# Kernel tuning notes

Measured on AMD Instinct MI355X. Metric: run time of the kernel, lower is better.

## Reference

```python
import jax, jax.numpy as jnp
import numpy as np

SEQ, B, CIN, H, K = 2048, 16, 512, 512, 2

def setup_inputs() -> dict:
    key = jax.random.key(0)
    k1, k2, k3 = jax.random.split(key, 3)
    x = jax.random.normal(k1, (SEQ, B, CIN), dtype=jnp.float32)
    W = jax.random.normal(k2, (3 * H, CIN, K), dtype=jnp.float32) * (1.0 / np.sqrt(CIN * K))
    b = jax.random.normal(k3, (3 * H,), dtype=jnp.float32) * 0.01
    return {"x": x, "W": W, "b": b}

def _qrnn_fo(x, W, b):
    # x: (T, B, Cin) -> conv input (B, Cin, T), causal left pad of K-1 zeros
    xb = jnp.transpose(x, (1, 2, 0))
    g = jax.lax.conv_general_dilated(
        xb, W, window_strides=(1,), padding=[(K - 1, 0)],
        dimension_numbers=("NCH", "OIH", "NCH"))
    g = g + b[None, :, None]
    g = jnp.transpose(g, (2, 0, 1))  # (T, B, 3H)
    zg, fg, og = jnp.split(g, 3, axis=-1)
    z = jnp.tanh(zg)
    f = jax.nn.sigmoid(fg)
    o = jax.nn.sigmoid(og)

    def step(c, gates_t):
        zt, ft, ot = gates_t
        c = ft * c + (1.0 - ft) * zt
        h = c * ot
        return c, h

    c0 = jnp.zeros((B, H), dtype=x.dtype)
    c_last, hs = jax.lax.scan(step, c0, (z, f, o))
    return hs, c_last

def reference(x, W, b):
    hs, c_last = _qrnn_fo(x, W, b)
    h_last = hs[-1]
    return hs, h_last[None, :], c_last[None, :]
```

## Files before the change

kernel.cpp:

```cpp
#include <hip/hip_runtime.h>

#define SEQ   2048
#define BATCH 16
#define CINCH 512
#define HDIM  512
#define NDIM  1536
#define TBM   (SEQ*BATCH)
#define KRED  1024
#define NCH   32
#define CHL   64
#define NCOL  8192

typedef unsigned short ushort_t;
typedef __bf16 bf16x8 __attribute__((ext_vector_type(8)));
typedef unsigned short u16x8 __attribute__((ext_vector_type(8)));
typedef float f32x4 __attribute__((ext_vector_type(4)));

__device__ __forceinline__ float bf2f(ushort_t u) {
    return __uint_as_float(((unsigned int)u) << 16);
}
__device__ __forceinline__ ushort_t f2bf(float x) {
    unsigned int u = __float_as_uint(x);
    unsigned int r = u + 0x7fffu + ((u >> 16) & 1u);
    return (ushort_t)(r >> 16);
}

__global__ void cast_x_kernel(const float* __restrict__ x, ushort_t* __restrict__ xb) {
    int i = blockIdx.x * 256 + threadIdx.x;
    int e = i * 4;
    ushort4 r;
    if (e < BATCH * CINCH) {
        r.x = 0; r.y = 0; r.z = 0; r.w = 0;
    } else {
        float4 v = *(const float4*)(x + (e - BATCH * CINCH));
        r.x = f2bf(v.x); r.y = f2bf(v.y); r.z = f2bf(v.z); r.w = f2bf(v.w);
    }
    *(ushort4*)(xb + e) = r;
}

__global__ void repack_w_kernel(const float* __restrict__ W, ushort_t* __restrict__ wb) {
    int i = blockIdx.x * 256 + threadIdx.x;
    int o  = i >> 10;
    int r  = i & 1023;
    int k  = r >> 9;
    int ci = r & 511;
    wb[i] = f2bf(W[o * 1024 + ci * 2 + k]);
}

__device__ __forceinline__ void load_lds_16B(const ushort_t* g, ushort_t* l) {
    auto* gp = reinterpret_cast<const __attribute__((address_space(1))) unsigned int*>(
        reinterpret_cast<uintptr_t>(g));
    auto* lp = reinterpret_cast<__attribute__((address_space(3))) unsigned int*>(
        reinterpret_cast<uintptr_t>(l));
    __builtin_amdgcn_global_load_lds(gp, lp, 16, 0, 0);
}

__global__ __launch_bounds__(256) void gemm_gates_kernel(
    const ushort_t* __restrict__ xb, const ushort_t* __restrict__ wb,
    const float* __restrict__ bias,
    ushort_t* __restrict__ zb, ushort_t* __restrict__ fb, ushort_t* __restrict__ ob) {

    __shared__ ushort_t smem[2 * 128 * 64];
    ushort_t* As = smem;
    ushort_t* Bs = smem + 128 * 64;

    const int tid  = threadIdx.x;
    const int w    = tid >> 6;
    const int lane = tid & 63;
    const int quad = lane >> 4;
    const int l15  = lane & 15;
    const int wm   = w & 1;
    const int wn   = w >> 1;
    const int mBase = blockIdx.x * 128;
    const int nBase = blockIdx.y * 128;

    const int srow = lane >> 3;
    const int scb  = lane & 7;

    f32x4 acc[4][4];
#pragma unroll
    for (int i = 0; i < 4; ++i)
#pragma unroll
        for (int j = 0; j < 4; ++j)
            acc[i][j] = (f32x4){0.f, 0.f, 0.f, 0.f};

    for (int kt = 0; kt < 16; ++kt) {
        __syncthreads();
        const long aOff = (kt < 8) ? (long)kt * 64 : (long)16 * 512 + (long)(kt - 8) * 64;
#pragma unroll
        for (int i = 0; i < 4; ++i) {
            const int row = w * 32 + i * 8 + srow;
            const int cbd = scb ^ (row & 7);
            const ushort_t* ga = xb + (long)(mBase + row) * 512 + aOff + cbd * 8;
            load_lds_16B(ga, &As[(w * 32 + i * 8) * 64]);
            const ushort_t* gb = wb + (long)(nBase + row) * 1024 + kt * 64 + cbd * 8;
            load_lds_16B(gb, &Bs[(w * 32 + i * 8) * 64]);
        }
        __syncthreads();

#pragma unroll
        for (int ks = 0; ks < 2; ++ks) {
            bf16x8 af[4], bfr[4];
            const int cbd = ks * 4 + quad;
#pragma unroll
            for (int mt = 0; mt < 4; ++mt) {
                int ml  = wm * 64 + mt * 16 + l15;
                int off = ml * 64 + ((cbd ^ (ml & 7)) * 8);
                af[mt] = __builtin_bit_cast(bf16x8, *(const u16x8*)(&As[off]));
            }
#pragma unroll
            for (int nt = 0; nt < 4; ++nt) {
                int nl  = wn * 64 + nt * 16 + l15;
                int off = nl * 64 + ((cbd ^ (nl & 7)) * 8);
                bfr[nt] = __builtin_bit_cast(bf16x8, *(const u16x8*)(&Bs[off]));
            }
#pragma unroll
            for (int mt = 0; mt < 4; ++mt)
#pragma unroll
                for (int nt = 0; nt < 4; ++nt)
                    acc[mt][nt] = __builtin_amdgcn_mfma_f32_16x16x32_bf16(
                        af[mt], bfr[nt], acc[mt][nt], 0, 0, 0);
        }
    }

    const int gate = nBase >> 9;
    const int hb   = nBase & 511;

    __syncthreads();
#pragma unroll
    for (int nt = 0; nt < 4; ++nt) {
        const int n_local = wn * 64 + nt * 16 + l15;
        const float bv = bias[nBase + n_local];
#pragma unroll
        for (int mt = 0; mt < 4; ++mt) {
#pragma unroll
            for (int r = 0; r < 4; ++r) {
                const int m_local = wm * 64 + mt * 16 + quad * 4 + r;
                float g = acc[mt][nt][r] + bv;
                float a;
                if (gate == 0) {
                    float e = __expf(-2.f * fabsf(g));
                    float t = (1.f - e) / (1.f + e);
                    a = copysignf(t, g);
                } else {
                    a = 1.f / (1.f + __expf(-g));
                }
                const int phys = ((n_local >> 3) ^ (m_local & 7)) * 8 + (n_local & 7);
                smem[m_local * 128 + phys] = f2bf(a);
            }
        }
    }
    __syncthreads();

    ushort_t* outp = (gate == 0) ? zb : (gate == 1) ? fb : ob;
#pragma unroll
    for (int s = 0; s < 8; ++s) {
        const int m_local = w * 32 + s * 4 + quad;
        const int blk = l15 ^ (m_local & 7);
        u16x8 v = *(const u16x8*)(&smem[m_local * 128 + blk * 8]);
        *(u16x8*)(outp + (long)(mBase + m_local) * 512 + hb + l15 * 8) = v;
    }
}

__global__ __launch_bounds__(256) void scan_compose(
    const ushort_t* __restrict__ zb, const ushort_t* __restrict__ fb,
    float* __restrict__ Acomp, float* __restrict__ Bcomp) {
    const int col = (blockIdx.x & 31) * 256 + threadIdx.x;
    const int ch  = blockIdx.x >> 5;
    const long base = (long)ch * CHL * NCOL + col;
    float A = 1.f, Bv = 0.f;
    const int U = 16;
    for (int w0 = 0; w0 < CHL; w0 += U) {
        float zc[U], fc[U];
#pragma unroll
        for (int u = 0; u < U; ++u) {
            long idx = base + (long)(w0 + u) * NCOL;
            zc[u] = bf2f(zb[idx]); fc[u] = bf2f(fb[idx]);
        }
#pragma unroll
        for (int u = 0; u < U; ++u) {
            Bv = fc[u] * Bv + (1.f - fc[u]) * zc[u];
            A *= fc[u];
        }
    }
    Acomp[ch * NCOL + col] = A;
    Bcomp[ch * NCOL + col] = Bv;
}

__global__ void scan_prefix(const float* __restrict__ Acomp,
                            const float* __restrict__ Bcomp,
                            float* __restrict__ Cin) {
    const int col = blockIdx.x * 256 + threadIdx.x;
    float c = 0.f;
#pragma unroll 4
    for (int ch = 0; ch < NCH; ++ch) {
        Cin[ch * NCOL + col] = c;
        c = Acomp[ch * NCOL + col] * c + Bcomp[ch * NCOL + col];
    }
}

__global__ __launch_bounds__(256) void scan_apply(
    const ushort_t* __restrict__ zb, const ushort_t* __restrict__ fb,
    const ushort_t* __restrict__ ob, const float* __restrict__ Cin,
    float* __restrict__ out) {
    const int col = (blockIdx.x & 31) * 256 + threadIdx.x;
    const int ch  = blockIdx.x >> 5;
    const long base = (long)ch * CHL * NCOL + col;
    float c = Cin[ch * NCOL + col];
    float h = 0.f;
    const int U = 16;
    for (int w0 = 0; w0 < CHL; w0 += U) {
        float zc[U], fc[U], oc[U];
#pragma unroll
        for (int u = 0; u < U; ++u) {
            long idx = base + (long)(w0 + u) * NCOL;
            zc[u] = bf2f(zb[idx]); fc[u] = bf2f(fb[idx]); oc[u] = bf2f(ob[idx]);
        }
#pragma unroll
        for (int u = 0; u < U; ++u) {
            c = fc[u] * c + (1.f - fc[u]) * zc[u];
            h = c * oc[u];
            out[base + (long)(w0 + u) * NCOL] = h;
        }
    }
    if (ch == NCH - 1) {
        out[(long)SEQ * NCOL + col] = h;
        out[(long)SEQ * NCOL + NCOL + col] = c;
    }
}

extern "C" void kernel_launch(void* const* d_in, const int* in_sizes, int n_in,
                              void* d_out, int out_size, void* d_ws, size_t ws_size,
                              hipStream_t stream) {
    const float* x  = (const float*)d_in[0];
    const float* W  = (const float*)d_in[1];
    const float* bi = (const float*)d_in[2];
    float* out = (float*)d_out;

    char* ws = (char*)d_ws;
    const size_t xbN = (size_t)(TBM + BATCH) * CINCH;
    const size_t wbN = (size_t)NDIM * KRED;
    const size_t gN  = (size_t)TBM * HDIM;
    ushort_t* xb = (ushort_t*)ws;
    ushort_t* wb = (ushort_t*)(ws + xbN * 2);
    ushort_t* zb = (ushort_t*)(ws + xbN * 2 + wbN * 2);
    ushort_t* fb = zb + gN;
    ushort_t* ob = fb + gN;
    float* Acomp = (float*)ws;
    float* Bcomp = Acomp + NCH * NCOL;
    float* Cin   = Bcomp + NCH * NCOL;

    cast_x_kernel<<<16392, 256, 0, stream>>>(x, xb);
    repack_w_kernel<<<6144, 256, 0, stream>>>(W, wb);
    dim3 ggrid(TBM / 128, NDIM / 128);
    gemm_gates_kernel<<<ggrid, 256, 0, stream>>>(xb, wb, bi, zb, fb, ob);
    scan_compose<<<NCH * 32, 256, 0, stream>>>(zb, fb, Acomp, Bcomp);
    scan_prefix<<<NCOL / 256, 256, 0, stream>>>(Acomp, Bcomp, Cin);
    scan_apply<<<NCH * 32, 256, 0, stream>>>(zb, fb, ob, Cin, out);
}
```

Measured before the change: 296.0 us.

## Restructure gate GEMM into 256x256 double-buffered pipelined tiles and vectorize scans

The gate GEMM moves from 128x128 tiles with 4 waves to 256x256 tiles with 8 waves. It double-buffers A and B in 128KB of dynamic LDS, splits each K-step into four MFMA phases separated by barriers and s_setprio, and issues the loads for the next tile while the current one computes. The block index is remapped so consecutive blocks share rows and improve L2 reuse. The scan compose and apply kernels now process 4 columns per thread with ushort4 and float4 accesses, which widens memory transactions. The cost is heavier register pressure (32 accumulators per lane), a large LDS footprint that limits occupancy, and fewer blocks in the scan kernels.

```diff
diff --git a/kernel.cpp b/kernel.cpp
--- a/kernel.cpp
+++ b/kernel.cpp
@@ -55,136 +55,201 @@
     __builtin_amdgcn_global_load_lds(gp, lp, 16, 0, 0);
 }
 
-__global__ __launch_bounds__(256) void gemm_gates_kernel(
+__device__ __forceinline__ bf16x8 frag(const ushort_t* buf, int row, int cb) {
+    return __builtin_bit_cast(bf16x8,
+        *(const u16x8*)(&buf[row * 64 + ((cb ^ (row & 7)) * 8)]));
+}
+
+#define PHASE_BAR() do { __builtin_amdgcn_s_barrier(); asm volatile("" ::: "memory"); } while (0)
+
+__global__ __launch_bounds__(512, 2) void gemm_gates_kernel(
     const ushort_t* __restrict__ xb, const ushort_t* __restrict__ wb,
     const float* __restrict__ bias,
     ushort_t* __restrict__ zb, ushort_t* __restrict__ fb, ushort_t* __restrict__ ob) {
 
-    __shared__ ushort_t smem[2 * 128 * 64];
-    ushort_t* As = smem;
-    ushort_t* Bs = smem + 128 * 64;
+    extern __shared__ ushort_t smem[];
 
     const int tid  = threadIdx.x;
     const int w    = tid >> 6;
     const int lane = tid & 63;
     const int quad = lane >> 4;
     const int l15  = lane & 15;
-    const int wm   = w & 1;
-    const int wn   = w >> 1;
-    const int mBase = blockIdx.x * 128;
-    const int nBase = blockIdx.y * 128;
-
-    const int srow = lane >> 3;
-    const int scb  = lane & 7;
-
-    f32x4 acc[4][4];
-#pragma unroll
-    for (int i = 0; i < 4; ++i)
+    const int wm   = w >> 2;
+    const int wn   = w & 3;
+
+    const int wg    = (blockIdx.x & 7) * 96 + (blockIdx.x >> 3);
+    const int mBase = (wg / 6) * 256;
+    const int nBase = (wg % 6) * 256;
+
+    const int r0    = tid >> 3;
+    const int cbd   = (tid & 7) ^ (r0 & 7);
+    const int wbase = w * 8;
+
+    auto stageA = [&](ushort_t* dst, int u) {
+        const long aoff = (u < 8) ? (long)u * 64 : 8192L + (long)(u - 8) * 64;
+#pragma unroll
+        for (int ra = 0; ra < 4; ++ra) {
+            load_lds_16B(xb + (long)(mBase + ra * 64 + r0) * 512 + aoff + cbd * 8,
+                         dst + (ra * 64 + wbase) * 64);
+        }
+    };
+    auto stageB = [&](ushort_t* dst, int u) {
+        const long koff = (long)u * 64;
+#pragma unroll
+        for (int ra = 0; ra < 4; ++ra) {
+            load_lds_16B(wb + (long)(nBase + ra * 64 + r0) * 1024 + koff + cbd * 8,
+                         dst + (ra * 64 + wbase) * 64);
+        }
+    };
+
+    f32x4 acc[8][4];
+#pragma unroll
+    for (int i = 0; i < 8; ++i)
 #pragma unroll
         for (int j = 0; j < 4; ++j)
             acc[i][j] = (f32x4){0.f, 0.f, 0.f, 0.f};
 
-    for (int kt = 0; kt < 16; ++kt) {
-        __syncthreads();
-        const long aOff = (kt < 8) ? (long)kt * 64 : (long)16 * 512 + (long)(kt - 8) * 64;
-#pragma unroll
-        for (int i = 0; i < 4; ++i) {
-            const int row = w * 32 + i * 8 + srow;
-            const int cbd = scb ^ (row & 7);
-            const ushort_t* ga = xb + (long)(mBase + row) * 512 + aOff + cbd * 8;
-            load_lds_16B(ga, &As[(w * 32 + i * 8) * 64]);
-            const ushort_t* gb = wb + (long)(nBase + row) * 1024 + kt * 64 + cbd * 8;
-            load_lds_16B(gb, &Bs[(w * 32 + i * 8) * 64]);
-        }
-        __syncthreads();
-
-#pragma unroll
-        for (int ks = 0; ks < 2; ++ks) {
-            bf16x8 af[4], bfr[4];
-            const int cbd = ks * 4 + quad;
-#pragma unroll
-            for (int mt = 0; mt < 4; ++mt) {
-                int ml  = wm * 64 + mt * 16 + l15;
-                int off = ml * 64 + ((cbd ^ (ml & 7)) * 8);
-                af[mt] = __builtin_bit_cast(bf16x8, *(const u16x8*)(&As[off]));
-            }
-#pragma unroll
-            for (int nt = 0; nt < 4; ++nt) {
-                int nl  = wn * 64 + nt * 16 + l15;
-                int off = nl * 64 + ((cbd ^ (nl & 7)) * 8);
-                bfr[nt] = __builtin_bit_cast(bf16x8, *(const u16x8*)(&Bs[off]));
-            }
-#pragma unroll
-            for (int mt = 0; mt < 4; ++mt)
-#pragma unroll
-                for (int nt = 0; nt < 4; ++nt)
-                    acc[mt][nt] = __builtin_amdgcn_mfma_f32_16x16x32_bf16(
-                        af[mt], bfr[nt], acc[mt][nt], 0, 0, 0);
-        }
+    stageA(smem, 0);
+    stageB(smem + 32768, 0);
+    stageB(smem + 49152, 1);
+    asm volatile("s_waitcnt vmcnt(4)" ::: "memory");
+    PHASE_BAR();
+
+    int cur = 0;
+    for (int t = 0; t < 16; ++t) {
+        const ushort_t* cA = smem + cur * 16384;
+        const ushort_t* cB = smem + 32768 + cur * 16384;
+        bf16x8 a[4], b[4];
+
+#pragma unroll
+        for (int mt = 0; mt < 4; ++mt) a[mt] = frag(cA, wm * 128 + mt * 16 + l15, quad);
+#pragma unroll
+        for (int nt = 0; nt < 4; ++nt) b[nt] = frag(cB, wn * 64 + nt * 16 + l15, quad);
+        if (t < 15) stageA(smem + (cur ^ 1) * 16384, t + 1);
+        __builtin_amdgcn_s_setprio(1);
+#pragma unroll
+        for (int mt = 0; mt < 4; ++mt)
+#pragma unroll
+            for (int nt = 0; nt < 4; ++nt)
+                acc[mt][nt] = __builtin_amdgcn_mfma_f32_16x16x32_bf16(a[mt], b[nt], acc[mt][nt], 0, 0, 0);
+        __builtin_amdgcn_s_setprio(0);
+        PHASE_BAR();
+
+#pragma unroll
+        for (int mt = 0; mt < 4; ++mt) a[mt] = frag(cA, wm * 128 + (mt + 4) * 16 + l15, quad);
+        __builtin_amdgcn_s_setprio(1);
+#pragma unroll
+        for (int mt = 0; mt < 4; ++mt)
+#pragma unroll
+            for (int nt = 0; nt < 4; ++nt)
+                acc[mt + 4][nt] = __builtin_amdgcn_mfma_f32_16x16x32_bf16(a[mt], b[nt], acc[mt + 4][nt], 0, 0, 0);
+        __builtin_amdgcn_s_setprio(0);
+        PHASE_BAR();
+
+#pragma unroll
+        for (int mt = 0; mt < 4; ++mt) a[mt] = frag(cA, wm * 128 + mt * 16 + l15, 4 + quad);
+#pragma unroll
+        for (int nt = 0; nt < 4; ++nt) b[nt] = frag(cB, wn * 64 + nt * 16 + l15, 4 + quad);
+        __builtin_amdgcn_s_setprio(1);
+#pragma unroll
+        for (int mt = 0; mt < 4; ++mt)
+#pragma unroll
+            for (int nt = 0; nt < 4; ++nt)
+                acc[mt][nt] = __builtin_amdgcn_mfma_f32_16x16x32_bf16(a[mt], b[nt], acc[mt][nt], 0, 0, 0);
+        __builtin_amdgcn_s_setprio(0);
+        PHASE_BAR();
+
+#pragma unroll
+        for (int mt = 0; mt < 4; ++mt) a[mt] = frag(cA, wm * 128 + (mt + 4) * 16 + l15, 4 + quad);
+        __builtin_amdgcn_s_setprio(1);
+#pragma unroll
+        for (int mt = 0; mt < 4; ++mt)
+#pragma unroll
+            for (int nt = 0; nt < 4; ++nt)
+                acc[mt + 4][nt] = __builtin_amdgcn_mfma_f32_16x16x32_bf16(a[mt], b[nt], acc[mt + 4][nt], 0, 0, 0);
+        __builtin_amdgcn_s_setprio(0);
+        if (t < 14) {
+            stageB(smem + 32768 + cur * 16384, t + 2);
+            asm volatile("s_waitcnt vmcnt(4)" ::: "memory");
+        } else {
+            asm volatile("s_waitcnt vmcnt(0)" ::: "memory");
+        }
+        PHASE_BAR();
+        cur ^= 1;
     }
 
     const int gate = nBase >> 9;
     const int hb   = nBase & 511;
 
-    __syncthreads();
 #pragma unroll
     for (int nt = 0; nt < 4; ++nt) {
         const int n_local = wn * 64 + nt * 16 + l15;
         const float bv = bias[nBase + n_local];
 #pragma unroll
-        for (int mt = 0; mt < 4; ++mt) {
+        for (int mt = 0; mt < 8; ++mt) {
 #pragma unroll
             for (int r = 0; r < 4; ++r) {
-                const int m_local = wm * 64 + mt * 16 + quad * 4 + r;
+                const int m_local = wm * 128 + mt * 16 + quad * 4 + r;
                 float g = acc[mt][nt][r] + bv;
-                float a;
+                float av;
                 if (gate == 0) {
                     float e = __expf(-2.f * fabsf(g));
-                    float t = (1.f - e) / (1.f + e);
-                    a = copysignf(t, g);
+                    float tt = (1.f - e) / (1.f + e);
+                    av = copysignf(tt, g);
                 } else {
-                    a = 1.f / (1.f + __expf(-g));
+                    av = 1.f / (1.f + __expf(-g));
                 }
                 const int phys = ((n_local >> 3) ^ (m_local & 7)) * 8 + (n_local & 7);
-                smem[m_local * 128 + phys] = f2bf(a);
+                smem[m_local * 256 + phys] = f2bf(av);
             }
         }
     }
     __syncthreads();
 
     ushort_t* outp = (gate == 0) ? zb : (gate == 1) ? fb : ob;
-#pragma unroll
-    for (int s = 0; s < 8; ++s) {
-        const int m_local = w * 32 + s * 4 + quad;
-        const int blk = l15 ^ (m_local & 7);
-        u16x8 v = *(const u16x8*)(&smem[m_local * 128 + blk * 8]);
-        *(u16x8*)(outp + (long)(mBase + m_local) * 512 + hb + l15 * 8) = v;
-    }
+    const int lb    = tid & 31;
+    const int mrow0 = tid >> 5;
+#pragma unroll
+    for (int s = 0; s < 16; ++s) {
+        const int m_local = s * 16 + mrow0;
+        u16x8 v = *(const u16x8*)(&smem[m_local * 256 + ((lb ^ (m_local & 7)) * 8)]);
+        *(u16x8*)(outp + (long)(mBase + m_local) * 512 + hb + lb * 8) = v;
+    }
+}
+
+__device__ __forceinline__ void scan_step(float z, float f, float& A, float& Bv) {
+    Bv = f * Bv + (1.f - f) * z;
+    A *= f;
 }
 
 __global__ __launch_bounds__(256) void scan_compose(
     const ushort_t* __restrict__ zb, const ushort_t* __restrict__ fb,
     float* __restrict__ Acomp, float* __restrict__ Bcomp) {
-    const int col = (blockIdx.x & 31) * 256 + threadIdx.x;
-    const int ch  = blockIdx.x >> 5;
+    const int cg  = (blockIdx.x & 7) * 256 + threadIdx.x;
+    const int ch  = blockIdx.x >> 3;
+    const int col = cg * 4;
     const long base = (long)ch * CHL * NCOL + col;
-    float A = 1.f, Bv = 0.f;
-    const int U = 16;
+    float Ax = 1.f, Ay = 1.f, Az = 1.f, Aw = 1.f;
+    float Bx = 0.f, By = 0.f, Bz = 0.f, Bw = 0.f;
+    const int U = 8;
     for (int w0 = 0; w0 < CHL; w0 += U) {
-        float zc[U], fc[U];
+        ushort4 zr[U], fr[U];
 #pragma unroll
         for (int u = 0; u < U; ++u) {
-            long idx = base + (long)(w0 + u) * NCOL;
-            zc[u] = bf2f(zb[idx]); fc[u] = bf2f(fb[idx]);
+            const long idx = base + (long)(w0 + u) * NCOL;
+            zr[u] = *(const ushort4*)(zb + idx);
+            fr[u] = *(const ushort4*)(fb + idx);
         }
 #pragma unroll
         for (int u = 0; u < U; ++u) {
-            Bv = fc[u] * Bv + (1.f - fc[u]) * zc[u];
-            A *= fc[u];
-        }
-    }
-    Acomp[ch * NCOL + col] = A;
-    Bcomp[ch * NCOL + col] = Bv;
+            scan_step(bf2f(zr[u].x), bf2f(fr[u].x), Ax, Bx);
+            scan_step(bf2f(zr[u].y), bf2f(fr[u].y), Ay, By);
+            scan_step(bf2f(zr[u].z), bf2f(fr[u].z), Az, Bz);
+            scan_step(bf2f(zr[u].w), bf2f(fr[u].w), Aw, Bw);
+        }
+    }
+    *(float4*)(Acomp + (long)ch * NCOL + col) = make_float4(Ax, Ay, Az, Aw);
+    *(float4*)(Bcomp + (long)ch * NCOL + col) = make_float4(Bx, By, Bz, Bw);
 }
 
 __global__ void scan_prefix(const float* __restrict__ Acomp,
@@ -203,29 +268,36 @@
     const ushort_t* __restrict__ zb, const ushort_t* __restrict__ fb,
     const ushort_t* __restrict__ ob, const float* __restrict__ Cin,
     float* __restrict__ out) {
-    const int col = (blockIdx.x & 31) * 256 + threadIdx.x;
-    const int ch  = blockIdx.x >> 5;
+    const int cg  = (blockIdx.x & 7) * 256 + threadIdx.x;
+    const int ch  = blockIdx.x >> 3;
+    const int col = cg * 4;
     const long base = (long)ch * CHL * NCOL + col;
-    float c = Cin[ch * NCOL + col];
-    float h = 0.f;
-    const int U = 16;
+    float4 c0 = *(const float4*)(Cin + (long)ch * NCOL + col);
+    float cx = c0.x, cy = c0.y, cz = c0.z, cw = c0.w;
+    float hx = 0.f, hy = 0.f, hz = 0.f, hw = 0.f;
+    const int U = 8;
     for (int w0 = 0; w0 < CHL; w0 += U) {
-        float zc[U], fc[U], oc[U];
+        ushort4 zr[U], fr[U], orr[U];
 #pragma unroll
         for (int u = 0; u < U; ++u) {
-            long idx = base + (long)(w0 + u) * NCOL;
-            zc[u] = bf2f(zb[idx]); fc[u] = bf2f(fb[idx]); oc[u] = bf2f(ob[idx]);
+            const long idx = base + (long)(w0 + u) * NCOL;
+            zr[u]  = *(const ushort4*)(zb + idx);
+            fr[u]  = *(const ushort4*)(fb + idx);
+            orr[u] = *(const ushort4*)(ob + idx);
         }
 #pragma unroll
         for (int u = 0; u < U; ++u) {
-            c = fc[u] * c + (1.f - fc[u]) * zc[u];
-            h = c * oc[u];
-            out[base + (long)(w0 + u) * NCOL] = h;
+            float f, z;
+            f = bf2f(fr[u].x); z = bf2f(zr[u].x); cx = f * cx + (1.f - f) * z; hx = cx * bf2f(orr[u].x);
+            f = bf2f(fr[u].y); z = bf2f(zr[u].y); cy = f * cy + (1.f - f) * z; hy = cy * bf2f(orr[u].y);
+            f = bf2f(fr[u].z); z = bf2f(zr[u].z); cz = f * cz + (1.f - f) * z; hz = cz * bf2f(orr[u].z);
+            f = bf2f(fr[u].w); z = bf2f(zr[u].w); cw = f * cw + (1.f - f) * z; hw = cw * bf2f(orr[u].w);
+            *(float4*)(out + base + (long)(w0 + u) * NCOL) = make_float4(hx, hy, hz, hw);
         }
     }
     if (ch == NCH - 1) {
-        out[(long)SEQ * NCOL + col] = h;
-        out[(long)SEQ * NCOL + NCOL + col] = c;
+        *(float4*)(out + (long)SEQ * NCOL + col)        = make_float4(hx, hy, hz, hw);
+        *(float4*)(out + (long)SEQ * NCOL + NCOL + col) = make_float4(cx, cy, cz, cw);
     }
 }
 
@@ -250,11 +322,17 @@
     float* Bcomp = Acomp + NCH * NCOL;
     float* Cin   = Bcomp + NCH * NCOL;
 
+    static bool s_attr_set = false;
+    if (!s_attr_set) {
+        (void)hipFuncSetAttribute(reinterpret_cast<const void*>(&gemm_gates_kernel),
+                                  hipFuncAttributeMaxDynamicSharedMemorySize, 131072);
+        s_attr_set = true;
+    }
+
     cast_x_kernel<<<16392, 256, 0, stream>>>(x, xb);
     repack_w_kernel<<<6144, 256, 0, stream>>>(W, wb);
-    dim3 ggrid(TBM / 128, NDIM / 128);
-    gemm_gates_kernel<<<ggrid, 256, 0, stream>>>(xb, wb, bi, zb, fb, ob);
-    scan_compose<<<NCH * 32, 256, 0, stream>>>(zb, fb, Acomp, Bcomp);
+    gemm_gates_kernel<<<dim3(768), 512, 131072, stream>>>(xb, wb, bi, zb, fb, ob);
+    scan_compose<<<NCH * 8, 256, 0, stream>>>(zb, fb, Acomp, Bcomp);
     scan_prefix<<<NCOL / 256, 256, 0, stream>>>(Acomp, Bcomp, Cin);
-    scan_apply<<<NCH * 32, 256, 0, stream>>>(zb, fb, ob, Cin, out);
-}
+    scan_apply<<<NCH * 8, 256, 0, stream>>>(zb, fb, ob, Cin, out);
+}
```

Result: no change. 291.2 us (-1.6%).

## Load GEMM B fragments directly to registers and vectorize scan kernels by four columns

Applied to the files above, without the earlier changes.

The GEMM no longer stages the weight tile in LDS. Each lane loads its B fragments straight from global memory into registers, double-buffered across pairs of K steps, and only the A tile goes through LDS. This is meant to halve LDS traffic and shared memory use, possibly raising occupancy, at the cost of more VGPRs and uncoalesced global reads for B. The scan compose and apply kernels now process four columns per thread with ushort4/float4 accesses to cut instruction count. This leaves only 256 blocks per scan kernel, which may underfill the GPU.

```diff
diff --git a/kernel.cpp b/kernel.cpp
--- a/kernel.cpp
+++ b/kernel.cpp
@@ -55,14 +55,17 @@
     __builtin_amdgcn_global_load_lds(gp, lp, 16, 0, 0);
 }
 
+__device__ __forceinline__ bf16x8 bload(const ushort_t* p) {
+    return __builtin_bit_cast(bf16x8, *(const u16x8*)(p));
+}
+
 __global__ __launch_bounds__(256) void gemm_gates_kernel(
     const ushort_t* __restrict__ xb, const ushort_t* __restrict__ wb,
     const float* __restrict__ bias,
     ushort_t* __restrict__ zb, ushort_t* __restrict__ fb, ushort_t* __restrict__ ob) {
 
-    __shared__ ushort_t smem[2 * 128 * 64];
+    __shared__ ushort_t smem[128 * 128];
     ushort_t* As = smem;
-    ushort_t* Bs = smem + 128 * 64;
 
     const int tid  = threadIdx.x;
     const int w    = tid >> 6;
@@ -77,6 +80,8 @@
     const int srow = lane >> 3;
     const int scb  = lane & 7;
 
+    const ushort_t* bbase = wb + (long)(nBase + wn * 64 + l15) * 1024 + quad * 8;
+
     f32x4 acc[4][4];
 #pragma unroll
     for (int i = 0; i < 4; ++i)
@@ -84,23 +89,35 @@
         for (int j = 0; j < 4; ++j)
             acc[i][j] = (f32x4){0.f, 0.f, 0.f, 0.f};
 
-    for (int kt = 0; kt < 16; ++kt) {
+    bf16x8 bc0[4], bc1[4], bn0[4], bn1[4];
+
+#pragma unroll
+    for (int nt = 0; nt < 4; ++nt) {
+        bc0[nt] = bload(bbase + nt * 16384);
+        bc1[nt] = bload(bbase + nt * 16384 + 32);
+    }
+
+    for (int kt = 0; kt < 16; kt += 2) {
         __syncthreads();
-        const long aOff = (kt < 8) ? (long)kt * 64 : (long)16 * 512 + (long)(kt - 8) * 64;
-#pragma unroll
-        for (int i = 0; i < 4; ++i) {
-            const int row = w * 32 + i * 8 + srow;
-            const int cbd = scb ^ (row & 7);
-            const ushort_t* ga = xb + (long)(mBase + row) * 512 + aOff + cbd * 8;
-            load_lds_16B(ga, &As[(w * 32 + i * 8) * 64]);
-            const ushort_t* gb = wb + (long)(nBase + row) * 1024 + kt * 64 + cbd * 8;
-            load_lds_16B(gb, &Bs[(w * 32 + i * 8) * 64]);
+        {
+            const long aOff = (kt < 8) ? (long)kt * 64 : (long)16 * 512 + (long)(kt - 8) * 64;
+#pragma unroll
+            for (int i = 0; i < 4; ++i) {
+                const int row = w * 32 + i * 8 + srow;
+                const int cbd = scb ^ (row & 7);
+                load_lds_16B(xb + (long)(mBase + row) * 512 + aOff + cbd * 8,
+                             &As[(w * 32 + i * 8) * 64]);
+            }
         }
         __syncthreads();
-
+#pragma unroll
+        for (int nt = 0; nt < 4; ++nt) {
+            bn0[nt] = bload(bbase + nt * 16384 + (kt + 1) * 64);
+            bn1[nt] = bload(bbase + nt * 16384 + (kt + 1) * 64 + 32);
+        }
 #pragma unroll
         for (int ks = 0; ks < 2; ++ks) {
-            bf16x8 af[4], bfr[4];
+            bf16x8 af[4];
             const int cbd = ks * 4 + quad;
 #pragma unroll
             for (int mt = 0; mt < 4; ++mt) {
@@ -109,17 +126,49 @@
                 af[mt] = __builtin_bit_cast(bf16x8, *(const u16x8*)(&As[off]));
             }
 #pragma unroll
-            for (int nt = 0; nt < 4; ++nt) {
-                int nl  = wn * 64 + nt * 16 + l15;
-                int off = nl * 64 + ((cbd ^ (nl & 7)) * 8);
-                bfr[nt] = __builtin_bit_cast(bf16x8, *(const u16x8*)(&Bs[off]));
-            }
-#pragma unroll
             for (int mt = 0; mt < 4; ++mt)
 #pragma unroll
                 for (int nt = 0; nt < 4; ++nt)
                     acc[mt][nt] = __builtin_amdgcn_mfma_f32_16x16x32_bf16(
-                        af[mt], bfr[nt], acc[mt][nt], 0, 0, 0);
+                        af[mt], (ks == 0) ? bc0[nt] : bc1[nt], acc[mt][nt], 0, 0, 0);
+        }
+
+        __syncthreads();
+        {
+            const int ko = kt + 1;
+            const long aOff = (ko < 8) ? (long)ko * 64 : (long)16 * 512 + (long)(ko - 8) * 64;
+#pragma unroll
+            for (int i = 0; i < 4; ++i) {
+                const int row = w * 32 + i * 8 + srow;
+                const int cbd = scb ^ (row & 7);
+                load_lds_16B(xb + (long)(mBase + row) * 512 + aOff + cbd * 8,
+                             &As[(w * 32 + i * 8) * 64]);
+            }
+        }
+        __syncthreads();
+        if (kt + 2 < 16) {
+#pragma unroll
+            for (int nt = 0; nt < 4; ++nt) {
+                bc0[nt] = bload(bbase + nt * 16384 + (kt + 2) * 64);
+                bc1[nt] = bload(bbase + nt * 16384 + (kt + 2) * 64 + 32);
+            }
+        }
+#pragma unroll
+        for (int ks = 0; ks < 2; ++ks) {
+            bf16x8 af[4];
+            const int cbd = ks * 4 + quad;
+#pragma unroll
+            for (int mt = 0; mt < 4; ++mt) {
+                int ml  = wm * 64 + mt * 16 + l15;
+                int off = ml * 64 + ((cbd ^ (ml & 7)) * 8);
+                af[mt] = __builtin_bit_cast(bf16x8, *(const u16x8*)(&As[off]));
+            }
+#pragma unroll
+            for (int mt = 0; mt < 4; ++mt)
+#pragma unroll
+                for (int nt = 0; nt < 4; ++nt)
+                    acc[mt][nt] = __builtin_amdgcn_mfma_f32_16x16x32_bf16(
+                        af[mt], (ks == 0) ? bn0[nt] : bn1[nt], acc[mt][nt], 0, 0, 0);
         }
     }
 
@@ -162,29 +211,39 @@
     }
 }
 
+__device__ __forceinline__ void scan_step(float z, float f, float& A, float& Bv) {
+    Bv = f * Bv + (1.f - f) * z;
+    A *= f;
+}
+
 __global__ __launch_bounds__(256) void scan_compose(
     const ushort_t* __restrict__ zb, const ushort_t* __restrict__ fb,
     float* __restrict__ Acomp, float* __restrict__ Bcomp) {
-    const int col = (blockIdx.x & 31) * 256 + threadIdx.x;
-    const int ch  = blockIdx.x >> 5;
+    const int cg  = (blockIdx.x & 7) * 256 + threadIdx.x;
+    const int ch  = blockIdx.x >> 3;
+    const int col = cg * 4;
     const long base = (long)ch * CHL * NCOL + col;
-    float A = 1.f, Bv = 0.f;
-    const int U = 16;
+    float Ax = 1.f, Ay = 1.f, Az = 1.f, Aw = 1.f;
+    float Bx = 0.f, By = 0.f, Bz = 0.f, Bw = 0.f;
+    const int U = 8;
     for (int w0 = 0; w0 < CHL; w0 += U) {
-        float zc[U], fc[U];
+        ushort4 zr[U], fr[U];
 #pragma unroll
         for (int u = 0; u < U; ++u) {
-            long idx = base + (long)(w0 + u) * NCOL;
-            zc[u] = bf2f(zb[idx]); fc[u] = bf2f(fb[idx]);
+            const long idx = base + (long)(w0 + u) * NCOL;
+            zr[u] = *(const ushort4*)(zb + idx);
+            fr[u] = *(const ushort4*)(fb + idx);
         }
 #pragma unroll
         for (int u = 0; u < U; ++u) {
-            Bv = fc[u] * Bv + (1.f - fc[u]) * zc[u];
-            A *= fc[u];
-        }
-    }
-    Acomp[ch * NCOL + col] = A;
-    Bcomp[ch * NCOL + col] = Bv;
+            scan_step(bf2f(zr[u].x), bf2f(fr[u].x), Ax, Bx);
+            scan_step(bf2f(zr[u].y), bf2f(fr[u].y), Ay, By);
+            scan_step(bf2f(zr[u].z), bf2f(fr[u].z), Az, Bz);
+            scan_step(bf2f(zr[u].w), bf2f(fr[u].w), Aw, Bw);
+        }
+    }
+    *(float4*)(Acomp + (long)ch * NCOL + col) = make_float4(Ax, Ay, Az, Aw);
+    *(float4*)(Bcomp + (long)ch * NCOL + col) = make_float4(Bx, By, Bz, Bw);
 }
 
 __global__ void scan_prefix(const float* __restrict__ Acomp,
@@ -203,29 +262,36 @@
     const ushort_t* __restrict__ zb, const ushort_t* __restrict__ fb,
     const ushort_t* __restrict__ ob, const float* __restrict__ Cin,
     float* __restrict__ out) {
-    const int col = (blockIdx.x & 31) * 256 + threadIdx.x;
-    const int ch  = blockIdx.x >> 5;
+    const int cg  = (blockIdx.x & 7) * 256 + threadIdx.x;
+    const int ch  = blockIdx.x >> 3;
+    const int col = cg * 4;
     const long base = (long)ch * CHL * NCOL + col;
-    float c = Cin[ch * NCOL + col];
-    float h = 0.f;
-    const int U = 16;
+    float4 c0 = *(const float4*)(Cin + (long)ch * NCOL + col);
+    float cx = c0.x, cy = c0.y, cz = c0.z, cw = c0.w;
+    float hx = 0.f, hy = 0.f, hz = 0.f, hw = 0.f;
+    const int U = 8;
     for (int w0 = 0; w0 < CHL; w0 += U) {
-        float zc[U], fc[U], oc[U];
+        ushort4 zr[U], fr[U], orr[U];
 #pragma unroll
         for (int u = 0; u < U; ++u) {
-            long idx = base + (long)(w0 + u) * NCOL;
-            zc[u] = bf2f(zb[idx]); fc[u] = bf2f(fb[idx]); oc[u] = bf2f(ob[idx]);
+            const long idx = base + (long)(w0 + u) * NCOL;
+            zr[u]  = *(const ushort4*)(zb + idx);
+            fr[u]  = *(const ushort4*)(fb + idx);
+            orr[u] = *(const ushort4*)(ob + idx);
         }
 #pragma unroll
         for (int u = 0; u < U; ++u) {
-            c = fc[u] * c + (1.f - fc[u]) * zc[u];
-            h = c * oc[u];
-            out[base + (long)(w0 + u) * NCOL] = h;
+            float f, z;
+            f = bf2f(fr[u].x); z = bf2f(zr[u].x); cx = f * cx + (1.f - f) * z; hx = cx * bf2f(orr[u].x);
+            f = bf2f(fr[u].y); z = bf2f(zr[u].y); cy = f * cy + (1.f - f) * z; hy = cy * bf2f(orr[u].y);
+            f = bf2f(fr[u].z); z = bf2f(zr[u].z); cz = f * cz + (1.f - f) * z; hz = cz * bf2f(orr[u].z);
+            f = bf2f(fr[u].w); z = bf2f(zr[u].w); cw = f * cw + (1.f - f) * z; hw = cw * bf2f(orr[u].w);
+            *(float4*)(out + base + (long)(w0 + u) * NCOL) = make_float4(hx, hy, hz, hw);
         }
     }
     if (ch == NCH - 1) {
-        out[(long)SEQ * NCOL + col] = h;
-        out[(long)SEQ * NCOL + NCOL + col] = c;
+        *(float4*)(out + (long)SEQ * NCOL + col)        = make_float4(hx, hy, hz, hw);
+        *(float4*)(out + (long)SEQ * NCOL + NCOL + col) = make_float4(cx, cy, cz, cw);
     }
 }
 
@@ -254,7 +320,7 @@
     repack_w_kernel<<<6144, 256, 0, stream>>>(W, wb);
     dim3 ggrid(TBM / 128, NDIM / 128);
     gemm_gates_kernel<<<ggrid, 256, 0, stream>>>(xb, wb, bi, zb, fb, ob);
-    scan_compose<<<NCH * 32, 256, 0, stream>>>(zb, fb, Acomp, Bcomp);
+    scan_compose<<<NCH * 8, 256, 0, stream>>>(zb, fb, Acomp, Bcomp);
     scan_prefix<<<NCOL / 256, 256, 0, stream>>>(Acomp, Bcomp, Cin);
-    scan_apply<<<NCH * 32, 256, 0, stream>>>(zb, fb, ob, Cin, out);
-}
+    scan_apply<<<NCH * 8, 256, 0, stream>>>(zb, fb, ob, Cin, out);
+}
```

Result: slower. 397.8 us (+34.4%).
